# Kernel tuning notes

Hardware: AMD Instinct MI355X
Metric: run time of the kernel (lower is better)

Reference implementation:

```python
import jax, jax.numpy as jnp
import numpy as np
from jax.scipy.special import logsumexp

BS, SEQ, DM = 4, 4096, 1024
H, HD = 16, 64
BLK = 128
NB = SEQ // BLK          # 32 blocks
MAX_NB = 32
N_ITERS = 5
TEMP = 1.0
CLIP = 1.0


def setup_inputs() -> dict:
    key = jax.random.key(0)
    ks = jax.random.split(key, 12)
    s = 0.02
    return {
        'inputs_q': jax.random.normal(ks[0], (BS, SEQ, DM), jnp.float32),
        'wq': jax.random.normal(ks[1], (DM, H, HD), jnp.float32) * s,
        'bq': jnp.zeros((H, HD), jnp.float32),
        'wk': jax.random.normal(ks[2], (DM, H, HD), jnp.float32) * s,
        'bk': jnp.zeros((H, HD), jnp.float32),
        'wv': jax.random.normal(ks[3], (DM, H, HD), jnp.float32) * s,
        'bv': jnp.zeros((H, HD), jnp.float32),
        'w_sort': jax.random.normal(ks[4], (H, HD, MAX_NB), jnp.float32) * s,
        'b_sort': jnp.zeros((MAX_NB,), jnp.float32),
        'wo': jax.random.normal(ks[5], (H, HD, DM), jnp.float32) * s,
        'bo': jnp.zeros((DM,), jnp.float32),
    }


def sinkhorn_operator(log_alpha, n_iters=N_ITERS, temp=TEMP, clip=CLIP):
    # non-causal path of the original: iterative row/col log-normalization
    n = log_alpha.shape[1]
    la = jnp.reshape(log_alpha, (-1, n, n)) / temp
    for _ in range(n_iters):
        la = la - logsumexp(la, axis=2, keepdims=True)  # row normalize
        la = la - logsumexp(la, axis=1, keepdims=True)  # col normalize
    return jnp.exp(jnp.clip(la, -clip, clip))


def reference(inputs_q, wq, bq, wk, bk, wv, bv, w_sort, b_sort, wo, bo):
    bs, qlen, _ = inputs_q.shape
    nb = qlen // BLK
    # QKV projections: (bs, seq, H, HD)
    q = jnp.einsum('bsf,fhd->bshd', inputs_q, wq) + bq
    k = jnp.einsum('bsf,fhd->bshd', inputs_q, wk) + bk  # self-attention: inputs_kv = inputs_q
    v = jnp.einsum('bsf,fhd->bshd', inputs_q, wv) + bv
    # block reshape: (bs, nb, BLK, H, HD)
    qb = q.reshape(bs, nb, BLK, H, HD)
    kb = k.reshape(bs, nb, BLK, H, HD)
    vb = v.reshape(bs, nb, BLK, H, HD)
    # sort network: pool keys within block, project (H,HD)->MAX_NB
    sum_key = jnp.sum(kb, axis=2)                                   # (bs, nb, H, HD)
    sort_out = jnp.einsum('bnhd,hdm->bnm', sum_key, w_sort) + b_sort
    sort_mat = sort_out[:, :, :nb]                                  # (bs, nb, nb)
    perm = sinkhorn_operator(sort_mat)                              # (bs, nb, nb)
    # soft block sorting of keys/values
    sorted_k = jnp.einsum('bnm,bmshd->bnshd', perm, kb)
    sorted_v = jnp.einsum('bnm,bmshd->bnshd', perm, vb)
    # attend within each block to [local kv ; sorted kv]
    kcat = jnp.concatenate([kb, sorted_k], axis=2)                  # (bs, nb, 2BLK, H, HD)
    vcat = jnp.concatenate([vb, sorted_v], axis=2)
    scale = 1.0 / jnp.sqrt(jnp.float32(HD))
    logits = jnp.einsum('bnqhd,bnkhd->bnhqk', qb * scale, kcat)     # (bs, nb, H, BLK, 2BLK)
    w = jax.nn.softmax(logits, axis=-1)
    x = jnp.einsum('bnhqk,bnkhd->bnqhd', w, vcat)                   # (bs, nb, BLK, H, HD)
    x = x.reshape(bs, qlen, H, HD)
    return jnp.einsum('bshd,hdf->bsf', x, wo) + bo
```

## Files before the change

### kernel.cpp

```cpp
#include <hip/hip_runtime.h>
#include <stdint.h>

typedef short bf16x8 __attribute__((ext_vector_type(8)));
typedef float f32x4 __attribute__((ext_vector_type(4)));
typedef unsigned short u16;
typedef unsigned short u16x4 __attribute__((ext_vector_type(4)));

#define AS1 __attribute__((address_space(1)))
#define AS3 __attribute__((address_space(3)))

__device__ __forceinline__ void gll16(const void* g, void* l) {
  __builtin_amdgcn_global_load_lds((const AS1 uint32_t*)g, (AS3 uint32_t*)l, 16, 0, 0);
}

__device__ __forceinline__ f32x4 mfma16(bf16x8 a, bf16x8 b, f32x4 c) {
  return __builtin_amdgcn_mfma_f32_16x16x32_bf16(a, b, c, 0, 0, 0);
}

__device__ __forceinline__ u16 f2bf(float f) {
  union { float f; uint32_t u; } c; c.f = f;
  uint32_t r = c.u + 0x7FFFu + ((c.u >> 16) & 1u);
  return (u16)(r >> 16);
}
__device__ __forceinline__ float bf2f(u16 h) {
  union { uint32_t u; float f; } c; c.u = ((uint32_t)h) << 16; return c.f;
}

__global__ __launch_bounds__(256) void k_cast(const float* __restrict__ in, u16* __restrict__ out) {
  int i = (blockIdx.x * 256 + threadIdx.x) * 4;
  float4 v = *(const float4*)(in + i);
  u16x4 r; r.x = f2bf(v.x); r.y = f2bf(v.y); r.z = f2bf(v.z); r.w = f2bf(v.w);
  *(u16x4*)(out + i) = r;
}

__global__ __launch_bounds__(1024) void k_transpose(const float* __restrict__ src, u16* __restrict__ dst,
                                                    int R, int C) {
  __shared__ float t[32][33];
  int tx = threadIdx.x, ty = threadIdx.y;
  t[ty][tx] = src[(size_t)(blockIdx.y * 32 + ty) * C + blockIdx.x * 32 + tx];
  __syncthreads();
  dst[(size_t)(blockIdx.x * 32 + ty) * R + blockIdx.y * 32 + tx] = f2bf(t[tx][ty]);
}

__global__ __launch_bounds__(256) void k_gemm_qkv(
    const u16* __restrict__ A, const u16* __restrict__ Bt,
    const float* __restrict__ bq, const float* __restrict__ bk, const float* __restrict__ bv,
    u16* __restrict__ Qb, u16* __restrict__ Kb, u16* __restrict__ Vbt)
{
  __shared__ u16 As[128 * 32];
  __shared__ u16 Bs[128 * 32];
  int tid = threadIdx.x, lane = tid & 63, w = tid >> 6;
  int wm = w >> 1, wn = w & 1;
  int m0 = blockIdx.y * 128, n0 = blockIdx.x * 128;

  int l4 = lane >> 2;
  int p = (lane & 3) ^ ((lane >> 3) & 3);
  const u16* Ag0 = A + (size_t)(m0 + w * 32 + l4) * 1024 + p * 8;
  const u16* Ag1 = A + (size_t)(m0 + w * 32 + 16 + l4) * 1024 + p * 8;
  const u16* Bg0 = Bt + (size_t)(n0 + w * 32 + l4) * 1024 + p * 8;
  const u16* Bg1 = Bt + (size_t)(n0 + w * 32 + 16 + l4) * 1024 + p * 8;
  u16* La0 = As + w * 1024; u16* La1 = As + w * 1024 + 512;
  u16* Lb0 = Bs + w * 1024; u16* Lb1 = Bs + w * 1024 + 512;

  int mm = lane & 15, quad = lane >> 4;
  int sw = quad ^ ((mm >> 1) & 3);
  const bf16x8* pa[4]; const bf16x8* pb[4];
#pragma unroll
  for (int t = 0; t < 4; ++t) {
    pa[t] = (const bf16x8*)(As + (wm * 64 + t * 16 + mm) * 32 + sw * 8);
    pb[t] = (const bf16x8*)(Bs + (wn * 64 + t * 16 + mm) * 32 + sw * 8);
  }

  f32x4 acc[4][4];
#pragma unroll
  for (int i = 0; i < 4; ++i)
#pragma unroll
    for (int j = 0; j < 4; ++j) acc[i][j] = (f32x4){0.f, 0.f, 0.f, 0.f};

  for (int kt = 0; kt < 32; ++kt) {
    int ko = kt * 32;
    gll16(Ag0 + ko, La0); gll16(Ag1 + ko, La1);
    gll16(Bg0 + ko, Lb0); gll16(Bg1 + ko, Lb1);
    __syncthreads();
    bf16x8 a[4], b[4];
#pragma unroll
    for (int t = 0; t < 4; ++t) { a[t] = *pa[t]; b[t] = *pb[t]; }
#pragma unroll
    for (int i = 0; i < 4; ++i)
#pragma unroll
      for (int j = 0; j < 4; ++j) acc[i][j] = mfma16(a[i], b[j], acc[i][j]);
    __syncthreads();
  }

  int sel = n0 >> 10;
  const float* bias = sel == 0 ? bq : (sel == 1 ? bk : bv);
  float scl = sel == 0 ? 0.125f : 1.0f;
#pragma unroll
  for (int j = 0; j < 4; ++j) {
    int ng = n0 + wn * 64 + j * 16 + mm;
    int h = (ng >> 6) & 15, d = ng & 63;
    float bval = bias[ng & 1023];
#pragma unroll
    for (int i = 0; i < 4; ++i)
#pragma unroll
      for (int r = 0; r < 4; ++r) {
        int mg = m0 + wm * 64 + i * 16 + quad * 4 + r;
        int b_ = mg >> 12, s = mg & 4095;
        float v = (acc[i][j][r] + bval) * scl;
        if (sel == 0)      Qb [((size_t)(b_ * 16 + h) * 4096 + s) * 64 + d] = f2bf(v);
        else if (sel == 1) Kb [((size_t)(b_ * 16 + h) * 4096 + s) * 64 + d] = f2bf(v);
        else               Vbt[((size_t)(b_ * 16 + h) * 64 + d) * 4096 + s] = f2bf(v);
      }
  }
}

__global__ __launch_bounds__(256) void k_gemm_out(
    const u16* __restrict__ A, const u16* __restrict__ Bt,
    const float* __restrict__ bo, float* __restrict__ out)
{
  __shared__ u16 As[128 * 32];
  __shared__ u16 Bs[128 * 32];
  int tid = threadIdx.x, lane = tid & 63, w = tid >> 6;
  int wm = w >> 1, wn = w & 1;
  int m0 = blockIdx.y * 128, n0 = blockIdx.x * 128;
  int l4 = lane >> 2;
  int p = (lane & 3) ^ ((lane >> 3) & 3);
  const u16* Ag0 = A + (size_t)(m0 + w * 32 + l4) * 1024 + p * 8;
  const u16* Ag1 = A + (size_t)(m0 + w * 32 + 16 + l4) * 1024 + p * 8;
  const u16* Bg0 = Bt + (size_t)(n0 + w * 32 + l4) * 1024 + p * 8;
  const u16* Bg1 = Bt + (size_t)(n0 + w * 32 + 16 + l4) * 1024 + p * 8;
  u16* La0 = As + w * 1024; u16* La1 = As + w * 1024 + 512;
  u16* Lb0 = Bs + w * 1024; u16* Lb1 = Bs + w * 1024 + 512;
  int mm = lane & 15, quad = lane >> 4;
  int sw = quad ^ ((mm >> 1) & 3);
  const bf16x8* pa[4]; const bf16x8* pb[4];
#pragma unroll
  for (int t = 0; t < 4; ++t) {
    pa[t] = (const bf16x8*)(As + (wm * 64 + t * 16 + mm) * 32 + sw * 8);
    pb[t] = (const bf16x8*)(Bs + (wn * 64 + t * 16 + mm) * 32 + sw * 8);
  }
  f32x4 acc[4][4];
#pragma unroll
  for (int i = 0; i < 4; ++i)
#pragma unroll
    for (int j = 0; j < 4; ++j) acc[i][j] = (f32x4){0.f, 0.f, 0.f, 0.f};
  for (int kt = 0; kt < 32; ++kt) {
    int ko = kt * 32;
    gll16(Ag0 + ko, La0); gll16(Ag1 + ko, La1);
    gll16(Bg0 + ko, Lb0); gll16(Bg1 + ko, Lb1);
    __syncthreads();
    bf16x8 a[4], b[4];
#pragma unroll
    for (int t = 0; t < 4; ++t) { a[t] = *pa[t]; b[t] = *pb[t]; }
#pragma unroll
    for (int i = 0; i < 4; ++i)
#pragma unroll
      for (int j = 0; j < 4; ++j) acc[i][j] = mfma16(a[i], b[j], acc[i][j]);
    __syncthreads();
  }
#pragma unroll
  for (int j = 0; j < 4; ++j) {
    int ng = n0 + wn * 64 + j * 16 + mm;
    float bval = bo[ng];
#pragma unroll
    for (int i = 0; i < 4; ++i)
#pragma unroll
      for (int r = 0; r < 4; ++r) {
        int mg = m0 + wm * 64 + i * 16 + quad * 4 + r;
        out[(size_t)mg * 1024 + ng] = acc[i][j][r] + bval;
      }
  }
}

__global__ __launch_bounds__(64) void k_sumkey(const u16* __restrict__ Kb, float* __restrict__ sumk) {
  int d = threadIdx.x, n = blockIdx.x, h = blockIdx.y, b = blockIdx.z;
  const u16* p = Kb + (((size_t)(b * 16 + h) * 4096) + n * 128) * 64 + d;
  float a0 = 0, a1 = 0, a2 = 0, a3 = 0;
  for (int s = 0; s < 128; s += 4) {
    a0 += bf2f(p[(s + 0) * 64]); a1 += bf2f(p[(s + 1) * 64]);
    a2 += bf2f(p[(s + 2) * 64]); a3 += bf2f(p[(s + 3) * 64]);
  }
  sumk[((size_t)(b * 32 + n) * 16 + h) * 64 + d] = (a0 + a1) + (a2 + a3);
}

__global__ __launch_bounds__(256) void k_sortmm(const float* __restrict__ sumk, const float* __restrict__ wsort,
                                                const float* __restrict__ bsort, float* __restrict__ so) {
  __shared__ float red[256];
  int n = blockIdx.x, b = blockIdx.y, t = threadIdx.x;
  int m = t & 31, kp = t >> 5;
  const float* row = sumk + (size_t)(b * 32 + n) * 1024;
  float acc = 0.f;
  for (int c = kp * 128; c < kp * 128 + 128; ++c) acc += row[c] * wsort[c * 32 + m];
  red[t] = acc;
  __syncthreads();
  if (t < 32) {
    float s = bsort[t];
#pragma unroll
    for (int q = 0; q < 8; ++q) s += red[q * 32 + t];
    so[(size_t)(b * 32 + n) * 32 + t] = s;
  }
}

__global__ __launch_bounds__(32) void k_sinkhorn(const float* __restrict__ so, float* __restrict__ perm) {
  __shared__ float A[32][33];
  int b = blockIdx.x, t = threadIdx.x;
  for (int i = 0; i < 32; ++i) A[i][t] = so[(size_t)(b * 32 + i) * 32 + t];
  __syncthreads();
  for (int it = 0; it < 5; ++it) {
    {
      float mx = -1e30f;
      for (int j = 0; j < 32; ++j) mx = fmaxf(mx, A[t][j]);
      float s = 0.f;
      for (int j = 0; j < 32; ++j) s += __expf(A[t][j] - mx);
      float l = mx + __logf(s);
      for (int j = 0; j < 32; ++j) A[t][j] -= l;
    }
    __syncthreads();
    {
      float mx = -1e30f;
      for (int j = 0; j < 32; ++j) mx = fmaxf(mx, A[j][t]);
      float s = 0.f;
      for (int j = 0; j < 32; ++j) s += __expf(A[j][t] - mx);
      float l = mx + __logf(s);
      for (int j = 0; j < 32; ++j) A[j][t] -= l;
    }
    __syncthreads();
  }
  for (int i = 0; i < 32; ++i)
    perm[(size_t)(b * 32 + i) * 32 + t] = __expf(fminf(fmaxf(A[i][t], -1.f), 1.f));
}

__global__ __launch_bounds__(256) void k_mix_k(
    const u16* __restrict__ Kb, const float* __restrict__ perm, u16* __restrict__ Ksort)
{
  __shared__ float P[32][32];
  int b = blockIdx.z, h = blockIdx.y, sg = blockIdx.x;
  int tid = threadIdx.x;
#pragma unroll
  for (int i = 0; i < 4; ++i) {
    int idx = i * 256 + tid;
    P[idx >> 5][idx & 31] = perm[b * 1024 + idx];
  }
  __syncthreads();
  int ss = sg * 4 + (tid >> 6), d = tid & 63;
  const u16* Kg = Kb + (size_t)(b * 16 + h) * 262144;
  float xk[32];
#pragma unroll
  for (int m = 0; m < 32; ++m) xk[m] = bf2f(Kg[(size_t)(m * 128 + ss) * 64 + d]);
  size_t tbase = (size_t)((b * 16 + h) * 32) * 8192;
#pragma unroll
  for (int nn = 0; nn < 32; ++nn) {
    float sk = 0.f;
#pragma unroll
    for (int m4 = 0; m4 < 8; ++m4) {
      float4 pv = *(const float4*)&P[nn][m4 * 4];
      sk += pv.x * xk[m4 * 4 + 0] + pv.y * xk[m4 * 4 + 1] + pv.z * xk[m4 * 4 + 2] + pv.w * xk[m4 * 4 + 3];
    }
    Ksort[tbase + (size_t)nn * 8192 + ss * 64 + d] = f2bf(sk);
  }
}

__global__ __launch_bounds__(256) void k_mix_v(
    const u16* __restrict__ Vbt, const float* __restrict__ perm, u16* __restrict__ Vsort)
{
  __shared__ float P[32][32];
  int b = blockIdx.z, h = blockIdx.y, dg = blockIdx.x;
  int tid = threadIdx.x;
#pragma unroll
  for (int i = 0; i < 4; ++i) {
    int idx = i * 256 + tid;
    P[idx >> 5][idx & 31] = perm[b * 1024 + idx];
  }
  __syncthreads();
  int d = dg * 2 + (tid >> 7), ss = tid & 127;
  const u16* Vg = Vbt + ((size_t)(b * 16 + h) * 64 + d) * 4096;
  float xv[32];
#pragma unroll
  for (int m = 0; m < 32; ++m) xv[m] = bf2f(Vg[m * 128 + ss]);
  size_t tbase = (size_t)((b * 16 + h) * 32) * 8192;
#pragma unroll
  for (int nn = 0; nn < 32; ++nn) {
    float sv = 0.f;
#pragma unroll
    for (int m4 = 0; m4 < 8; ++m4) {
      float4 pv = *(const float4*)&P[nn][m4 * 4];
      sv += pv.x * xv[m4 * 4 + 0] + pv.y * xv[m4 * 4 + 1] + pv.z * xv[m4 * 4 + 2] + pv.w * xv[m4 * 4 + 3];
    }
    Vsort[tbase + (size_t)nn * 8192 + d * 128 + ss] = f2bf(sv);
  }
}

__global__ __launch_bounds__(256, 2) void k_attn(
    const u16* __restrict__ Qb, const u16* __restrict__ Kb, const u16* __restrict__ Ksort,
    const u16* __restrict__ Vbt, const u16* __restrict__ Vsort, u16* __restrict__ X)
{
  __shared__ u16 Ks[16384];
  __shared__ u16 Vlo[8192];
  __shared__ u16 Vhi[8192];
  int tid = threadIdx.x, lane = tid & 63, w = tid >> 6;
  int n = blockIdx.x, h = blockIdx.y, b = blockIdx.z;
  size_t bh = (size_t)(b * 16 + h);
  size_t tileK = bh * 32 + n;

  {
    int l8 = lane >> 3, sl8 = lane & 7;
    const u16* Korig = Kb + (bh * 4096 + (size_t)n * 128) * 64;
    const u16* Ksrt  = Ksort + tileK * 8192;
#pragma unroll
    for (int c = 0; c < 8; ++c) {
      int cc = w * 8 + c;
      int r = cc * 8 + l8;
      int pk = sl8 ^ (r & 7);
      const u16* src = (cc < 16) ? (Korig + (size_t)r * 64 + pk * 8)
                                 : (Ksrt + (size_t)(r - 128) * 64 + pk * 8);
      gll16(src, Ks + cc * 512);
    }
    int l16 = lane >> 4, sl16 = lane & 15;
    const u16* Vorig = Vbt + bh * 262144 + (size_t)n * 128;
    const u16* Vsrt  = Vsort + tileK * 8192;
#pragma unroll
    for (int c = 0; c < 4; ++c) {
      int cc = w * 4 + c;
      int d = cc * 4 + l16;
      int pv = sl16 ^ (d & 15);
      gll16(Vorig + (size_t)d * 4096 + pv * 8, Vlo + cc * 512);
      gll16(Vsrt + (size_t)d * 128 + pv * 8, Vhi + cc * 512);
    }
  }

  int mm = lane & 15, quad = lane >> 4;
  bf16x8 qf[2][2];
  {
    size_t qrow = bh * 4096 + n * 128 + w * 32;
#pragma unroll
    for (int mt = 0; mt < 2; ++mt)
#pragma unroll
      for (int ks = 0; ks < 2; ++ks)
        qf[mt][ks] = *(const bf16x8*)(Qb + (qrow + mt * 16 + mm) * 64 + ks * 32 + quad * 8);
  }
  __syncthreads();

  f32x4 S[2][16];
#pragma unroll
  for (int mt = 0; mt < 2; ++mt)
#pragma unroll
    for (int nt = 0; nt < 16; ++nt) S[mt][nt] = (f32x4){0.f, 0.f, 0.f, 0.f};
#pragma unroll
  for (int nt = 0; nt < 16; ++nt) {
    int kk = nt * 16 + mm;
#pragma unroll
    for (int ks = 0; ks < 2; ++ks) {
      int ch = (ks * 4 + quad) ^ (kk & 7);
      bf16x8 bk = *(const bf16x8*)(Ks + kk * 64 + ch * 8);
      S[0][nt] = mfma16(qf[0][ks], bk, S[0][nt]);
      S[1][nt] = mfma16(qf[1][ks], bk, S[1][nt]);
    }
  }

  float mx[2][4], ls[2][4];
#pragma unroll
  for (int mt = 0; mt < 2; ++mt)
#pragma unroll
    for (int r = 0; r < 4; ++r) {
      float v = S[mt][0][r];
#pragma unroll
      for (int nt = 1; nt < 16; ++nt) v = fmaxf(v, S[mt][nt][r]);
#pragma unroll
      for (int o = 1; o < 16; o <<= 1) v = fmaxf(v, __shfl_xor(v, o));
      mx[mt][r] = v;
    }
#pragma unroll
  for (int mt = 0; mt < 2; ++mt)
#pragma unroll
    for (int nt = 0; nt < 16; ++nt)
#pragma unroll
      for (int r = 0; r < 4; ++r)
        S[mt][nt][r] = __expf(S[mt][nt][r] - mx[mt][r]);
#pragma unroll
  for (int mt = 0; mt < 2; ++mt)
#pragma unroll
    for (int r = 0; r < 4; ++r) {
      float s = 0.f;
#pragma unroll
      for (int nt = 0; nt < 16; ++nt) s += S[mt][nt][r];
#pragma unroll
      for (int o = 1; o < 16; o <<= 1) s += __shfl_xor(s, o);
      ls[mt][r] = s;
    }

  __syncthreads();

  u16* Pw = Ks + w * 4096;
  f32x4 O[2][4];
#pragma unroll
  for (int mt = 0; mt < 2; ++mt)
#pragma unroll
    for (int dt = 0; dt < 4; ++dt) O[mt][dt] = (f32x4){0.f, 0.f, 0.f, 0.f};

#pragma unroll
  for (int half = 0; half < 2; ++half) {
    const u16* Vp = half == 0 ? Vlo : Vhi;
#pragma unroll
    for (int mt = 0; mt < 2; ++mt)
#pragma unroll
      for (int nt8 = 0; nt8 < 8; ++nt8) {
        int nt = half * 8 + nt8;
        int kkl = nt8 * 16 + mm;
#pragma unroll
        for (int r = 0; r < 4; ++r) {
          int q = mt * 16 + quad * 4 + r;
          int ch = (kkl >> 3) ^ (q & 15);
          Pw[q * 128 + ch * 8 + (kkl & 7)] = f2bf(S[mt][nt][r]);
        }
      }
#pragma unroll
    for (int ksl = 0; ksl < 4; ++ksl) {
      bf16x8 pa[2];
#pragma unroll
      for (int mt = 0; mt < 2; ++mt) {
        int q = mt * 16 + mm;
        int ch = (ksl * 4 + quad) ^ (q & 15);
        pa[mt] = *(const bf16x8*)(Pw + q * 128 + ch * 8);
      }
#pragma unroll
      for (int dt = 0; dt < 4; ++dt) {
        int d = dt * 16 + mm;
        int ch = (ksl * 4 + quad) ^ (d & 15);
        bf16x8 vb = *(const bf16x8*)(Vp + d * 128 + ch * 8);
        O[0][dt] = mfma16(pa[0], vb, O[0][dt]);
        O[1][dt] = mfma16(pa[1], vb, O[1][dt]);
      }
    }
  }

#pragma unroll
  for (int mt = 0; mt < 2; ++mt)
#pragma unroll
    for (int dt = 0; dt < 4; ++dt)
#pragma unroll
      for (int r = 0; r < 4; ++r) {
        int q = w * 32 + mt * 16 + quad * 4 + r;
        float val = O[mt][dt][r] / ls[mt][r];
        size_t row = (size_t)b * 4096 + n * 128 + q;
        X[row * 1024 + h * 64 + dt * 16 + mm] = f2bf(val);
      }
}

extern "C" void kernel_launch(void* const* d_in, const int* in_sizes, int n_in,
                              void* d_out, int out_size, void* d_ws, size_t ws_size,
                              hipStream_t stream) {
  const float* inq   = (const float*)d_in[0];
  const float* wq    = (const float*)d_in[1];
  const float* bq    = (const float*)d_in[2];
  const float* wk    = (const float*)d_in[3];
  const float* bk    = (const float*)d_in[4];
  const float* wv    = (const float*)d_in[5];
  const float* bv    = (const float*)d_in[6];
  const float* wsort = (const float*)d_in[7];
  const float* bsort = (const float*)d_in[8];
  const float* wo    = (const float*)d_in[9];
  const float* bo    = (const float*)d_in[10];
  float* out = (float*)d_out;

  char* ws = (char*)d_ws;
  size_t off = 0;
  auto alloc = [&](size_t bytes) { char* p = ws + off; off += (bytes + 255) & ~(size_t)255; return p; };
  u16*  Qb    = (u16*)alloc(33554432);
  u16*  Kb    = (u16*)alloc(33554432);
  u16*  Vbt   = (u16*)alloc(33554432);
  u16*  Ksort = (u16*)alloc(33554432);
  u16*  Vsort = (u16*)alloc(33554432);
  u16*  Abf   = (u16*)alloc(33554432);
  u16*  Wqkvt = (u16*)alloc(6291456);
  u16*  Wot   = (u16*)alloc(2097152);
  float* sumk = (float*)alloc(524288);
  float* so   = (float*)alloc(16384);
  float* perm = (float*)alloc(16384);
  u16*  X = Abf;

  k_cast<<<16384, 256, 0, stream>>>(inq, Abf);
  dim3 tb(32, 32);
  k_transpose<<<dim3(32, 32), tb, 0, stream>>>(wq, Wqkvt,                   1024, 1024);
  k_transpose<<<dim3(32, 32), tb, 0, stream>>>(wk, Wqkvt + 1024 * 1024,     1024, 1024);
  k_transpose<<<dim3(32, 32), tb, 0, stream>>>(wv, Wqkvt + 2 * 1024 * 1024, 1024, 1024);
  k_transpose<<<dim3(32, 32), tb, 0, stream>>>(wo, Wot,                     1024, 1024);
  k_gemm_qkv<<<dim3(24, 128), 256, 0, stream>>>(Abf, Wqkvt, bq, bk, bv, Qb, Kb, Vbt);
  k_sumkey<<<dim3(32, 16, 4), 64, 0, stream>>>(Kb, sumk);
  k_sortmm<<<dim3(32, 4), 256, 0, stream>>>(sumk, wsort, bsort, so);
  k_sinkhorn<<<4, 32, 0, stream>>>(so, perm);
  k_mix_k<<<dim3(32, 16, 4), 256, 0, stream>>>(Kb, perm, Ksort);
  k_mix_v<<<dim3(32, 16, 4), 256, 0, stream>>>(Vbt, perm, Vsort);
  k_attn<<<dim3(32, 16, 4), 256, 0, stream>>>(Qb, Kb, Ksort, Vbt, Vsort, X);
  k_gemm_out<<<dim3(8, 128), 256, 0, stream>>>(X, Wot, bo, out);
}
```

Baseline: 523.9 us.

## Deepen GEMM K-tile, fuse key sum into QKV GEMM, merge small launches

The QKV and output GEMMs now load 64-wide K slices per barrier instead of 32, using a new XOR swizzle, which halves the number of sync rounds. The per-block key sum is computed in the QKV GEMM epilogue from the fp32 accumulators with shuffles and a shared-memory reduction, so the separate sumkey kernel and its re-read of K are gone. The four weight transposes become one launch, and the K and V mixing kernels become one launch. The costs are more shared memory per block and an extra barrier in the K-column blocks. The key sum now comes from unrounded fp32 values rather than the bf16-rounded K, which changes numerics slightly.

```diff
diff --git a/kernel.cpp b/kernel.cpp
--- a/kernel.cpp
+++ b/kernel.cpp
@@ -33,62 +33,72 @@
   *(u16x4*)(out + i) = r;
 }
 
-__global__ __launch_bounds__(1024) void k_transpose(const float* __restrict__ src, u16* __restrict__ dst,
-                                                    int R, int C) {
+__global__ __launch_bounds__(1024) void k_transpose4(
+    const float* __restrict__ wq, const float* __restrict__ wk,
+    const float* __restrict__ wv, const float* __restrict__ wo,
+    u16* __restrict__ Wqkvt, u16* __restrict__ Wot) {
   __shared__ float t[32][33];
+  const float* src; u16* dst;
+  int z = blockIdx.z;
+  if (z == 0)      { src = wq; dst = Wqkvt; }
+  else if (z == 1) { src = wk; dst = Wqkvt + 1024 * 1024; }
+  else if (z == 2) { src = wv; dst = Wqkvt + 2 * 1024 * 1024; }
+  else             { src = wo; dst = Wot; }
   int tx = threadIdx.x, ty = threadIdx.y;
-  t[ty][tx] = src[(size_t)(blockIdx.y * 32 + ty) * C + blockIdx.x * 32 + tx];
+  t[ty][tx] = src[(size_t)(blockIdx.y * 32 + ty) * 1024 + blockIdx.x * 32 + tx];
   __syncthreads();
-  dst[(size_t)(blockIdx.x * 32 + ty) * R + blockIdx.y * 32 + tx] = f2bf(t[tx][ty]);
+  dst[(size_t)(blockIdx.x * 32 + ty) * 1024 + blockIdx.y * 32 + tx] = f2bf(t[tx][ty]);
 }
 
 __global__ __launch_bounds__(256) void k_gemm_qkv(
     const u16* __restrict__ A, const u16* __restrict__ Bt,
     const float* __restrict__ bq, const float* __restrict__ bk, const float* __restrict__ bv,
-    u16* __restrict__ Qb, u16* __restrict__ Kb, u16* __restrict__ Vbt)
+    u16* __restrict__ Qb, u16* __restrict__ Kb, u16* __restrict__ Vbt, float* __restrict__ sumk)
 {
-  __shared__ u16 As[128 * 32];
-  __shared__ u16 Bs[128 * 32];
+  __shared__ u16 As[128 * 64];
+  __shared__ u16 Bs[128 * 64];
   int tid = threadIdx.x, lane = tid & 63, w = tid >> 6;
   int wm = w >> 1, wn = w & 1;
   int m0 = blockIdx.y * 128, n0 = blockIdx.x * 128;
 
-  int l4 = lane >> 2;
-  int p = (lane & 3) ^ ((lane >> 3) & 3);
-  const u16* Ag0 = A + (size_t)(m0 + w * 32 + l4) * 1024 + p * 8;
-  const u16* Ag1 = A + (size_t)(m0 + w * 32 + 16 + l4) * 1024 + p * 8;
-  const u16* Bg0 = Bt + (size_t)(n0 + w * 32 + l4) * 1024 + p * 8;
-  const u16* Bg1 = Bt + (size_t)(n0 + w * 32 + 16 + l4) * 1024 + p * 8;
-  u16* La0 = As + w * 1024; u16* La1 = As + w * 1024 + 512;
-  u16* Lb0 = Bs + w * 1024; u16* Lb1 = Bs + w * 1024 + 512;
+  int l8 = lane >> 3, sl8 = lane & 7;
+  int pg = sl8 ^ l8;
+  const u16* Ag[4]; const u16* Bg[4]; u16* La[4]; u16* Lb[4];
+#pragma unroll
+  for (int c = 0; c < 4; ++c) {
+    int cc = w * 4 + c, row = cc * 8 + l8;
+    Ag[c] = A + (size_t)(m0 + row) * 1024 + pg * 8;
+    Bg[c] = Bt + (size_t)(n0 + row) * 1024 + pg * 8;
+    La[c] = As + cc * 512;
+    Lb[c] = Bs + cc * 512;
+  }
 
   int mm = lane & 15, quad = lane >> 4;
-  int sw = quad ^ ((mm >> 1) & 3);
-  const bf16x8* pa[4]; const bf16x8* pb[4];
-#pragma unroll
-  for (int t = 0; t < 4; ++t) {
-    pa[t] = (const bf16x8*)(As + (wm * 64 + t * 16 + mm) * 32 + sw * 8);
-    pb[t] = (const bf16x8*)(Bs + (wn * 64 + t * 16 + mm) * 32 + sw * 8);
-  }
-
   f32x4 acc[4][4];
 #pragma unroll
   for (int i = 0; i < 4; ++i)
 #pragma unroll
     for (int j = 0; j < 4; ++j) acc[i][j] = (f32x4){0.f, 0.f, 0.f, 0.f};
 
-  for (int kt = 0; kt < 32; ++kt) {
-    int ko = kt * 32;
-    gll16(Ag0 + ko, La0); gll16(Ag1 + ko, La1);
-    gll16(Bg0 + ko, Lb0); gll16(Bg1 + ko, Lb1);
-    __syncthreads();
-    bf16x8 a[4], b[4];
-#pragma unroll
-    for (int t = 0; t < 4; ++t) { a[t] = *pa[t]; b[t] = *pb[t]; }
-#pragma unroll
-    for (int i = 0; i < 4; ++i)
-#pragma unroll
-      for (int j = 0; j < 4; ++j) acc[i][j] = mfma16(a[i], b[j], acc[i][j]);
+  for (int kt = 0; kt < 16; ++kt) {
+    int ko = kt * 64;
+#pragma unroll
+    for (int c = 0; c < 4; ++c) { gll16(Ag[c] + ko, La[c]); gll16(Bg[c] + ko, Lb[c]); }
+    __syncthreads();
+#pragma unroll
+    for (int ks = 0; ks < 2; ++ks) {
+      bf16x8 a[4], b[4];
+#pragma unroll
+      for (int t = 0; t < 4; ++t) {
+        int ch = (ks * 4 + quad) ^ (mm & 7);
+        a[t] = *(const bf16x8*)(As + (wm * 64 + t * 16 + mm) * 64 + ch * 8);
+        b[t] = *(const bf16x8*)(Bs + (wn * 64 + t * 16 + mm) * 64 + ch * 8);
+      }
+#pragma unroll
+      for (int i = 0; i < 4; ++i)
+#pragma unroll
+        for (int j = 0; j < 4; ++j) acc[i][j] = mfma16(a[i], b[j], acc[i][j]);
+    }
     __syncthreads();
   }
 
@@ -112,50 +122,80 @@
         else               Vbt[((size_t)(b_ * 16 + h) * 64 + d) * 4096 + s] = f2bf(v);
       }
   }
+
+  if (sel == 1) {
+    float cs[4];
+#pragma unroll
+    for (int j = 0; j < 4; ++j) {
+      int ng = n0 + wn * 64 + j * 16 + mm;
+      float bval = bias[ng & 1023];
+      float s = 16.f * bval;
+#pragma unroll
+      for (int i = 0; i < 4; ++i)
+#pragma unroll
+        for (int r = 0; r < 4; ++r) s += acc[i][j][r];
+      s += __shfl_xor(s, 16);
+      s += __shfl_xor(s, 32);
+      cs[j] = s;
+    }
+    float* red = (float*)As;
+    if (quad == 0) {
+#pragma unroll
+      for (int j = 0; j < 4; ++j) red[wm * 128 + wn * 64 + j * 16 + mm] = cs[j];
+    }
+    __syncthreads();
+    if (tid < 128) {
+      int b_ = m0 >> 12, n = (m0 >> 7) & 31;
+      sumk[(size_t)(b_ * 32 + n) * 1024 + (n0 - 1024) + tid] = red[tid] + red[128 + tid];
+    }
+  }
 }
 
 __global__ __launch_bounds__(256) void k_gemm_out(
     const u16* __restrict__ A, const u16* __restrict__ Bt,
     const float* __restrict__ bo, float* __restrict__ out)
 {
-  __shared__ u16 As[128 * 32];
-  __shared__ u16 Bs[128 * 32];
+  __shared__ u16 As[128 * 64];
+  __shared__ u16 Bs[128 * 64];
   int tid = threadIdx.x, lane = tid & 63, w = tid >> 6;
   int wm = w >> 1, wn = w & 1;
   int m0 = blockIdx.y * 128, n0 = blockIdx.x * 128;
-  int l4 = lane >> 2;
-  int p = (lane & 3) ^ ((lane >> 3) & 3);
-  const u16* Ag0 = A + (size_t)(m0 + w * 32 + l4) * 1024 + p * 8;
-  const u16* Ag1 = A + (size_t)(m0 + w * 32 + 16 + l4) * 1024 + p * 8;
-  const u16* Bg0 = Bt + (size_t)(n0 + w * 32 + l4) * 1024 + p * 8;
-  const u16* Bg1 = Bt + (size_t)(n0 + w * 32 + 16 + l4) * 1024 + p * 8;
-  u16* La0 = As + w * 1024; u16* La1 = As + w * 1024 + 512;
-  u16* Lb0 = Bs + w * 1024; u16* Lb1 = Bs + w * 1024 + 512;
+  int l8 = lane >> 3, sl8 = lane & 7;
+  int pg = sl8 ^ l8;
+  const u16* Ag[4]; const u16* Bg[4]; u16* La[4]; u16* Lb[4];
+#pragma unroll
+  for (int c = 0; c < 4; ++c) {
+    int cc = w * 4 + c, row = cc * 8 + l8;
+    Ag[c] = A + (size_t)(m0 + row) * 1024 + pg * 8;
+    Bg[c] = Bt + (size_t)(n0 + row) * 1024 + pg * 8;
+    La[c] = As + cc * 512;
+    Lb[c] = Bs + cc * 512;
+  }
   int mm = lane & 15, quad = lane >> 4;
-  int sw = quad ^ ((mm >> 1) & 3);
-  const bf16x8* pa[4]; const bf16x8* pb[4];
-#pragma unroll
-  for (int t = 0; t < 4; ++t) {
-    pa[t] = (const bf16x8*)(As + (wm * 64 + t * 16 + mm) * 32 + sw * 8);
-    pb[t] = (const bf16x8*)(Bs + (wn * 64 + t * 16 + mm) * 32 + sw * 8);
-  }
   f32x4 acc[4][4];
 #pragma unroll
   for (int i = 0; i < 4; ++i)
 #pragma unroll
     for (int j = 0; j < 4; ++j) acc[i][j] = (f32x4){0.f, 0.f, 0.f, 0.f};
-  for (int kt = 0; kt < 32; ++kt) {
-    int ko = kt * 32;
-    gll16(Ag0 + ko, La0); gll16(Ag1 + ko, La1);
-    gll16(Bg0 + ko, Lb0); gll16(Bg1 + ko, Lb1);
-    __syncthreads();
-    bf16x8 a[4], b[4];
-#pragma unroll
-    for (int t = 0; t < 4; ++t) { a[t] = *pa[t]; b[t] = *pb[t]; }
-#pragma unroll
-    for (int i = 0; i < 4; ++i)
-#pragma unroll
-      for (int j = 0; j < 4; ++j) acc[i][j] = mfma16(a[i], b[j], acc[i][j]);
+  for (int kt = 0; kt < 16; ++kt) {
+    int ko = kt * 64;
+#pragma unroll
+    for (int c = 0; c < 4; ++c) { gll16(Ag[c] + ko, La[c]); gll16(Bg[c] + ko, Lb[c]); }
+    __syncthreads();
+#pragma unroll
+    for (int ks = 0; ks < 2; ++ks) {
+      bf16x8 a[4], b[4];
+#pragma unroll
+      for (int t = 0; t < 4; ++t) {
+        int ch = (ks * 4 + quad) ^ (mm & 7);
+        a[t] = *(const bf16x8*)(As + (wm * 64 + t * 16 + mm) * 64 + ch * 8);
+        b[t] = *(const bf16x8*)(Bs + (wn * 64 + t * 16 + mm) * 64 + ch * 8);
+      }
+#pragma unroll
+      for (int i = 0; i < 4; ++i)
+#pragma unroll
+        for (int j = 0; j < 4; ++j) acc[i][j] = mfma16(a[i], b[j], acc[i][j]);
+    }
     __syncthreads();
   }
 #pragma unroll
@@ -170,17 +210,6 @@
         out[(size_t)mg * 1024 + ng] = acc[i][j][r] + bval;
       }
   }
-}
-
-__global__ __launch_bounds__(64) void k_sumkey(const u16* __restrict__ Kb, float* __restrict__ sumk) {
-  int d = threadIdx.x, n = blockIdx.x, h = blockIdx.y, b = blockIdx.z;
-  const u16* p = Kb + (((size_t)(b * 16 + h) * 4096) + n * 128) * 64 + d;
-  float a0 = 0, a1 = 0, a2 = 0, a3 = 0;
-  for (int s = 0; s < 128; s += 4) {
-    a0 += bf2f(p[(s + 0) * 64]); a1 += bf2f(p[(s + 1) * 64]);
-    a2 += bf2f(p[(s + 2) * 64]); a3 += bf2f(p[(s + 3) * 64]);
-  }
-  sumk[((size_t)(b * 32 + n) * 16 + h) * 64 + d] = (a0 + a1) + (a2 + a3);
 }
 
 __global__ __launch_bounds__(256) void k_sortmm(const float* __restrict__ sumk, const float* __restrict__ wsort,
@@ -230,11 +259,12 @@
     perm[(size_t)(b * 32 + i) * 32 + t] = __expf(fminf(fmaxf(A[i][t], -1.f), 1.f));
 }
 
-__global__ __launch_bounds__(256) void k_mix_k(
-    const u16* __restrict__ Kb, const float* __restrict__ perm, u16* __restrict__ Ksort)
+__global__ __launch_bounds__(256) void k_mix(
+    const u16* __restrict__ Kb, const u16* __restrict__ Vbt, const float* __restrict__ perm,
+    u16* __restrict__ Ksort, u16* __restrict__ Vsort)
 {
   __shared__ float P[32][32];
-  int b = blockIdx.z, h = blockIdx.y, sg = blockIdx.x;
+  int b = blockIdx.z, y = blockIdx.y, xg = blockIdx.x;
   int tid = threadIdx.x;
 #pragma unroll
   for (int i = 0; i < 4; ++i) {
@@ -242,51 +272,42 @@
     P[idx >> 5][idx & 31] = perm[b * 1024 + idx];
   }
   __syncthreads();
-  int ss = sg * 4 + (tid >> 6), d = tid & 63;
-  const u16* Kg = Kb + (size_t)(b * 16 + h) * 262144;
-  float xk[32];
-#pragma unroll
-  for (int m = 0; m < 32; ++m) xk[m] = bf2f(Kg[(size_t)(m * 128 + ss) * 64 + d]);
-  size_t tbase = (size_t)((b * 16 + h) * 32) * 8192;
-#pragma unroll
-  for (int nn = 0; nn < 32; ++nn) {
-    float sk = 0.f;
-#pragma unroll
-    for (int m4 = 0; m4 < 8; ++m4) {
-      float4 pv = *(const float4*)&P[nn][m4 * 4];
-      sk += pv.x * xk[m4 * 4 + 0] + pv.y * xk[m4 * 4 + 1] + pv.z * xk[m4 * 4 + 2] + pv.w * xk[m4 * 4 + 3];
-    }
-    Ksort[tbase + (size_t)nn * 8192 + ss * 64 + d] = f2bf(sk);
-  }
-}
-
-__global__ __launch_bounds__(256) void k_mix_v(
-    const u16* __restrict__ Vbt, const float* __restrict__ perm, u16* __restrict__ Vsort)
-{
-  __shared__ float P[32][32];
-  int b = blockIdx.z, h = blockIdx.y, dg = blockIdx.x;
-  int tid = threadIdx.x;
-#pragma unroll
-  for (int i = 0; i < 4; ++i) {
-    int idx = i * 256 + tid;
-    P[idx >> 5][idx & 31] = perm[b * 1024 + idx];
-  }
-  __syncthreads();
-  int d = dg * 2 + (tid >> 7), ss = tid & 127;
-  const u16* Vg = Vbt + ((size_t)(b * 16 + h) * 64 + d) * 4096;
-  float xv[32];
-#pragma unroll
-  for (int m = 0; m < 32; ++m) xv[m] = bf2f(Vg[m * 128 + ss]);
-  size_t tbase = (size_t)((b * 16 + h) * 32) * 8192;
-#pragma unroll
-  for (int nn = 0; nn < 32; ++nn) {
-    float sv = 0.f;
-#pragma unroll
-    for (int m4 = 0; m4 < 8; ++m4) {
-      float4 pv = *(const float4*)&P[nn][m4 * 4];
-      sv += pv.x * xv[m4 * 4 + 0] + pv.y * xv[m4 * 4 + 1] + pv.z * xv[m4 * 4 + 2] + pv.w * xv[m4 * 4 + 3];
-    }
-    Vsort[tbase + (size_t)nn * 8192 + d * 128 + ss] = f2bf(sv);
+  if (y < 16) {
+    int h = y;
+    int ss = xg * 4 + (tid >> 6), d = tid & 63;
+    const u16* Kg = Kb + (size_t)(b * 16 + h) * 262144;
+    float xk[32];
+#pragma unroll
+    for (int m = 0; m < 32; ++m) xk[m] = bf2f(Kg[(size_t)(m * 128 + ss) * 64 + d]);
+    size_t tbase = (size_t)((b * 16 + h) * 32) * 8192;
+#pragma unroll
+    for (int nn = 0; nn < 32; ++nn) {
+      float sk = 0.f;
+#pragma unroll
+      for (int m4 = 0; m4 < 8; ++m4) {
+        float4 pv = *(const float4*)&P[nn][m4 * 4];
+        sk += pv.x * xk[m4 * 4 + 0] + pv.y * xk[m4 * 4 + 1] + pv.z * xk[m4 * 4 + 2] + pv.w * xk[m4 * 4 + 3];
+      }
+      Ksort[tbase + (size_t)nn * 8192 + ss * 64 + d] = f2bf(sk);
+    }
+  } else {
+    int h = y - 16;
+    int d = xg * 2 + (tid >> 7), ss = tid & 127;
+    const u16* Vg = Vbt + ((size_t)(b * 16 + h) * 64 + d) * 4096;
+    float xv[32];
+#pragma unroll
+    for (int m = 0; m < 32; ++m) xv[m] = bf2f(Vg[m * 128 + ss]);
+    size_t tbase = (size_t)((b * 16 + h) * 32) * 8192;
+#pragma unroll
+    for (int nn = 0; nn < 32; ++nn) {
+      float sv = 0.f;
+#pragma unroll
+      for (int m4 = 0; m4 < 8; ++m4) {
+        float4 pv = *(const float4*)&P[nn][m4 * 4];
+        sv += pv.x * xv[m4 * 4 + 0] + pv.y * xv[m4 * 4 + 1] + pv.z * xv[m4 * 4 + 2] + pv.w * xv[m4 * 4 + 3];
+      }
+      Vsort[tbase + (size_t)nn * 8192 + d * 128 + ss] = f2bf(sv);
+    }
   }
 }
 
@@ -479,17 +500,11 @@
   u16*  X = Abf;
 
   k_cast<<<16384, 256, 0, stream>>>(inq, Abf);
-  dim3 tb(32, 32);
-  k_transpose<<<dim3(32, 32), tb, 0, stream>>>(wq, Wqkvt,                   1024, 1024);
-  k_transpose<<<dim3(32, 32), tb, 0, stream>>>(wk, Wqkvt + 1024 * 1024,     1024, 1024);
-  k_transpose<<<dim3(32, 32), tb, 0, stream>>>(wv, Wqkvt + 2 * 1024 * 1024, 1024, 1024);
-  k_transpose<<<dim3(32, 32), tb, 0, stream>>>(wo, Wot,                     1024, 1024);
-  k_gemm_qkv<<<dim3(24, 128), 256, 0, stream>>>(Abf, Wqkvt, bq, bk, bv, Qb, Kb, Vbt);
-  k_sumkey<<<dim3(32, 16, 4), 64, 0, stream>>>(Kb, sumk);
+  k_transpose4<<<dim3(32, 32, 4), dim3(32, 32), 0, stream>>>(wq, wk, wv, wo, Wqkvt, Wot);
+  k_gemm_qkv<<<dim3(24, 128), 256, 0, stream>>>(Abf, Wqkvt, bq, bk, bv, Qb, Kb, Vbt, sumk);
   k_sortmm<<<dim3(32, 4), 256, 0, stream>>>(sumk, wsort, bsort, so);
   k_sinkhorn<<<4, 32, 0, stream>>>(so, perm);
-  k_mix_k<<<dim3(32, 16, 4), 256, 0, stream>>>(Kb, perm, Ksort);
-  k_mix_v<<<dim3(32, 16, 4), 256, 0, stream>>>(Vbt, perm, Vsort);
+  k_mix<<<dim3(32, 32, 4), 256, 0, stream>>>(Kb, Vbt, perm, Ksort, Vsort);
   k_attn<<<dim3(32, 16, 4), 256, 0, stream>>>(Qb, Kb, Ksort, Vbt, Vsort, X);
   k_gemm_out<<<dim3(8, 128), 256, 0, stream>>>(X, Wot, bo, out);
 }
```

Measured after the change: 501.9 us. 1.04x faster.
